# Kernel tuning notes

Hardware: AMD Instinct MI355X
Metric: run time of the kernel (lower is better)

Reference implementation:

```python
import jax, jax.numpy as jnp
import numpy as np

N_NODES = 100000

def _sage_conv(x, src, dst, W_l, b_l, W_r):
    # PyG SAGEConv(aggr='mean'): out = lin_l(mean_{j in N(i)} x_j) + lin_r(x_i)
    agg = jax.ops.segment_sum(x[src], dst, num_segments=N_NODES)          # [N, F]
    cnt = jax.ops.segment_sum(jnp.ones_like(dst, dtype=x.dtype), dst,
                              num_segments=N_NODES)                        # [N]
    mean = agg / jnp.maximum(cnt, 1.0)[:, None]
    return mean @ W_l + b_l + x @ W_r

def setup_inputs() -> dict:
    key = jax.random.key(0)
    ks = jax.random.split(key, 10)
    F_in, H = 128, 16
    E, P = 1600000, 2000000
    x = jax.random.normal(ks[0], (N_NODES, F_in), dtype=jnp.float32)
    edge_index = jax.random.randint(ks[1], (2, E), 0, N_NODES, dtype=jnp.int64)
    decode_index = jax.random.randint(ks[2], (2, P), 0, N_NODES, dtype=jnp.int64)
    s1 = 1.0 / np.sqrt(F_in)
    s2 = 1.0 / np.sqrt(H)
    W1l = jax.random.uniform(ks[3], (F_in, H), jnp.float32, -s1, s1)
    b1 = jax.random.uniform(ks[4], (H,), jnp.float32, -s1, s1)
    W1r = jax.random.uniform(ks[5], (F_in, H), jnp.float32, -s1, s1)
    W2l = jax.random.uniform(ks[6], (H, H), jnp.float32, -s2, s2)
    b2 = jax.random.uniform(ks[7], (H,), jnp.float32, -s2, s2)
    W2r = jax.random.uniform(ks[8], (H, H), jnp.float32, -s2, s2)
    return {"x": x, "W1l": W1l, "b1": b1, "W1r": W1r,
            "W2l": W2l, "b2": b2, "W2r": W2r,
            "edge_index": edge_index, "decode_index": decode_index}

def reference(x, W1l, b1, W1r, W2l, b2, W2r, edge_index, decode_index):
    src, dst = edge_index[0], edge_index[1]
    h = _sage_conv(x, src, dst, W1l, b1, W1r)          # conv1
    h = jax.nn.relu(h)                                  # relu (dropout: eval -> identity)
    h = _sage_conv(h, src, dst, W2l, b2, W2r)           # conv2
    logits = jnp.sum(h[decode_index[0]] * h[decode_index[1]], axis=1)  # [P]
    return jax.nn.sigmoid(logits)
```

## Files before the change

### kernel.cpp

```cpp
#include <hip/hip_runtime.h>
#include <hip/hip_fp16.h>

#define N_NODES 100000
#define F_IN 128
#define H 16
#define NBIN 1563
#define BINCAP 1280
#define ECHUNK 8192
#define QSCALE 4096.0f
#define QINV (1.0f / 4096.0f)

__device__ inline unsigned int packi16(float a, float b) {
  int ia = __float2int_rn(fminf(fmaxf(a * QSCALE, -32767.f), 32767.f));
  int ib = __float2int_rn(fminf(fmaxf(b * QSCALE, -32767.f), 32767.f));
  return (unsigned int)((ia & 0xffff) | (ib << 16));
}

__device__ inline unsigned long long pk64(unsigned int w) {
  return ((unsigned long long)((w >> 16) ^ 0x8000u) << 32)
       | (unsigned long long)((w & 0xffffu) ^ 0x8000u);
}

__global__ void __launch_bounds__(512) k_init(int* __restrict__ binCur) {
  int i = blockIdx.x * 512 + threadIdx.x;
  if (i < NBIN) binCur[i] = i * BINCAP;
}

__global__ void __launch_bounds__(512) k_front(
    const float* __restrict__ x, const float* __restrict__ W1l,
    const float* __restrict__ W1r, unsigned short* __restrict__ y1l,
    float* __restrict__ y1r,
    const int* __restrict__ src, const int* __restrict__ dst,
    int* __restrict__ binCur, int* __restrict__ recs, int E, int fillB) {
  __shared__ __align__(16) char smem[49152];
  int t = threadIdx.x;
  int b = blockIdx.x;
  if (b < fillB) {
    int* hist = (int*)smem;
    int* gbase = hist + NBIN;
    int* cnt2 = gbase + NBIN;
    for (int bb = t; bb < NBIN; bb += 512) { hist[bb] = 0; cnt2[bb] = 0; }
    __syncthreads();
    int base = b * ECHUNK;
    int rec[16], bin[16];
#pragma unroll
    for (int j = 0; j < 16; ++j) {
      int e = base + j * 512 + t;
      if (e < E) {
        int s = src[e];
        int d = dst[e];
        rec[j] = (s << 6) | (d & 63);
        bin[j] = d >> 6;
        atomicAdd(&hist[bin[j]], 1);
      } else {
        bin[j] = -1;
      }
    }
    __syncthreads();
    for (int bb = t; bb < NBIN; bb += 512) {
      int c = hist[bb];
      if (c > 0) gbase[bb] = atomicAdd(&binCur[bb], c);
    }
    __syncthreads();
#pragma unroll
    for (int j = 0; j < 16; ++j) {
      if (bin[j] >= 0) {
        int loc = atomicAdd(&cnt2[bin[j]], 1);
        int slot = gbase[bin[j]] + loc;
        if (slot < (bin[j] + 1) * BINCAP)
          recs[slot] = rec[j];
      }
    }
  } else {
    int lb = b - fillB;
    int wid = __builtin_amdgcn_readfirstlane(t >> 6);
    int part = wid & 3;
    int g = wid >> 2;
    int ln = t & 63;
    int n = lb * 128 + g * 64 + ln;
    int nc = (n < N_NODES) ? n : (N_NODES - 1);
    float* red = (float*)smem + g * 6144;
    const float4* xr = (const float4*)(x + (size_t)nc * F_IN + part * (F_IN / 4));
    float4 xv[8];
#pragma unroll
    for (int j = 0; j < 8; ++j) xv[j] = xr[j];
    const float* Wl = W1l + part * (F_IN / 4) * H;
    const float* Wr = W1r + part * (F_IN / 4) * H;
    float al[H], ar[H];
#pragma unroll
    for (int c = 0; c < H; ++c) { al[c] = 0.f; ar[c] = 0.f; }
#pragma unroll
    for (int j = 0; j < 8; ++j) {
      float xs[4] = {xv[j].x, xv[j].y, xv[j].z, xv[j].w};
#pragma unroll
      for (int jj = 0; jj < 4; ++jj) {
        int k = j * 4 + jj;
#pragma unroll
        for (int c = 0; c < H; ++c) {
          al[c] = fmaf(xs[jj], Wl[k * H + c], al[c]);
          ar[c] = fmaf(xs[jj], Wr[k * H + c], ar[c]);
        }
      }
    }
    if (part != 0) {
      int base = (part - 1) * 2048;
#pragma unroll
      for (int c = 0; c < H; ++c) {
        red[base + c * 64 + ln] = al[c];
        red[base + (H + c) * 64 + ln] = ar[c];
      }
    }
    __syncthreads();
    if (part == 0 && n < N_NODES) {
#pragma unroll
      for (int c = 0; c < H; ++c) {
        al[c] = ((al[c] + red[c * 64 + ln]) + red[2048 + c * 64 + ln])
                + red[4096 + c * 64 + ln];
        ar[c] = ((ar[c] + red[(H + c) * 64 + ln]) + red[2048 + (H + c) * 64 + ln])
                + red[4096 + (H + c) * 64 + ln];
      }
      uint4 w0, w1;
      w0.x = packi16(al[0], al[1]);  w0.y = packi16(al[2], al[3]);
      w0.z = packi16(al[4], al[5]);  w0.w = packi16(al[6], al[7]);
      w1.x = packi16(al[8], al[9]);  w1.y = packi16(al[10], al[11]);
      w1.z = packi16(al[12], al[13]); w1.w = packi16(al[14], al[15]);
      uint4* ol = (uint4*)(y1l + (size_t)n * H);
      ol[0] = w0;
      ol[1] = w1;
      float4* orr = (float4*)(y1r + (size_t)n * H);
#pragma unroll
      for (int q = 0; q < 4; ++q)
        orr[q] = make_float4(ar[4 * q], ar[4 * q + 1], ar[4 * q + 2], ar[4 * q + 3]);
    }
  }
}

__global__ void __launch_bounds__(512) k_agg1(
    const int* __restrict__ recs, const int* __restrict__ binCur,
    const unsigned short* __restrict__ y1l, const float* __restrict__ y1r,
    const float* __restrict__ b1, const float* __restrict__ W2l,
    const float* __restrict__ W2r, unsigned short* __restrict__ z2l,
    float* __restrict__ z2r) {
  __shared__ unsigned long long acc[8][64];
  __shared__ int cnt[64];
  __shared__ float hf[16][64];
  __shared__ float w2l[256];
  __shared__ float w2r[256];
  int t = threadIdx.x;
  int b = blockIdx.x;
  ((unsigned long long*)acc)[t] = 0ULL;
  if (t < 64) cnt[t] = 0;
  if (t < 256) w2l[t] = W2l[t];
  else         w2r[t - 256] = W2r[t - 256];
  __syncthreads();
  int rbase = b * BINCAP;
  int R = binCur[b] - rbase;
  if (R > BINCAP) R = BINCAP;
  int rc[3];
  uint4 va[3], vb[3];
#pragma unroll
  for (int j = 0; j < 3; ++j) {
    int idx = j * 512 + t;
    rc[j] = (idx < R) ? recs[rbase + idx] : -1;
  }
#pragma unroll
  for (int j = 0; j < 3; ++j) {
    int s = (rc[j] >= 0) ? (rc[j] >> 6) : 0;
    const uint4* yp = (const uint4*)(y1l + (size_t)s * H);
    va[j] = yp[0];
    vb[j] = yp[1];
  }
#pragma unroll
  for (int j = 0; j < 3; ++j) {
    if (rc[j] >= 0) {
      int nb = rc[j] & 63;
      atomicAdd(&cnt[nb], 1);
      atomicAdd(&acc[0][nb], pk64(va[j].x));
      atomicAdd(&acc[1][nb], pk64(va[j].y));
      atomicAdd(&acc[2][nb], pk64(va[j].z));
      atomicAdd(&acc[3][nb], pk64(va[j].w));
      atomicAdd(&acc[4][nb], pk64(vb[j].x));
      atomicAdd(&acc[5][nb], pk64(vb[j].y));
      atomicAdd(&acc[6][nb], pk64(vb[j].z));
      atomicAdd(&acc[7][nb], pk64(vb[j].w));
    }
  }
  __syncthreads();
  int node = t >> 3;
  int q = t & 7;
  int n = b * 64 + node;
  float h0 = 0.f, h1 = 0.f;
  if (n < N_NODES) {
    int dg = cnt[node];
    unsigned int bias = (unsigned int)dg << 15;
    float s = QINV / fmaxf((float)dg, 1.f);
    float2 yr = *(const float2*)(y1r + (size_t)n * H + 2 * q);
    float2 bb = *(const float2*)(b1 + 2 * q);
    unsigned long long a = acc[q][node];
    int i0 = (int)((unsigned int)a - bias);
    int i1 = (int)((unsigned int)(a >> 32) - bias);
    h0 = fmaxf(fmaf((float)i0, s, bb.x + yr.x), 0.f);
    h1 = fmaxf(fmaf((float)i1, s, bb.y + yr.y), 0.f);
  }
  hf[2 * q][node] = h0;
  hf[2 * q + 1][node] = h1;
  __syncthreads();
  float zl0 = 0.f, zl1 = 0.f, zr0 = 0.f, zr1 = 0.f;
#pragma unroll
  for (int k = 0; k < 16; ++k) {
    float hk = hf[k][node];
    zl0 = fmaf(hk, w2l[k * 16 + 2 * q], zl0);
    zl1 = fmaf(hk, w2l[k * 16 + 2 * q + 1], zl1);
    zr0 = fmaf(hk, w2r[k * 16 + 2 * q], zr0);
    zr1 = fmaf(hk, w2r[k * 16 + 2 * q + 1], zr1);
  }
  if (n < N_NODES) {
    *(unsigned int*)(z2l + (size_t)n * H + 2 * q) = packi16(zl0, zl1);
    *(float2*)(z2r + (size_t)n * H + 2 * q) = make_float2(zr0, zr1);
  }
}

__global__ void __launch_bounds__(512) k_agg2(
    const int* __restrict__ recs, const int* __restrict__ binCur,
    const unsigned short* __restrict__ z2l, const float* __restrict__ z2r,
    const float* __restrict__ b2, __half* __restrict__ h2) {
  __shared__ unsigned long long acc[8][64];
  __shared__ int cnt[64];
  int t = threadIdx.x;
  int b = blockIdx.x;
  ((unsigned long long*)acc)[t] = 0ULL;
  if (t < 64) cnt[t] = 0;
  __syncthreads();
  int rbase = b * BINCAP;
  int R = binCur[b] - rbase;
  if (R > BINCAP) R = BINCAP;
  int rc[3];
  uint4 va[3], vb[3];
#pragma unroll
  for (int j = 0; j < 3; ++j) {
    int idx = j * 512 + t;
    rc[j] = (idx < R) ? recs[rbase + idx] : -1;
  }
#pragma unroll
  for (int j = 0; j < 3; ++j) {
    int s = (rc[j] >= 0) ? (rc[j] >> 6) : 0;
    const uint4* yp = (const uint4*)(z2l + (size_t)s * H);
    va[j] = yp[0];
    vb[j] = yp[1];
  }
#pragma unroll
  for (int j = 0; j < 3; ++j) {
    if (rc[j] >= 0) {
      int nb = rc[j] & 63;
      atomicAdd(&cnt[nb], 1);
      atomicAdd(&acc[0][nb], pk64(va[j].x));
      atomicAdd(&acc[1][nb], pk64(va[j].y));
      atomicAdd(&acc[2][nb], pk64(va[j].z));
      atomicAdd(&acc[3][nb], pk64(va[j].w));
      atomicAdd(&acc[4][nb], pk64(vb[j].x));
      atomicAdd(&acc[5][nb], pk64(vb[j].y));
      atomicAdd(&acc[6][nb], pk64(vb[j].z));
      atomicAdd(&acc[7][nb], pk64(vb[j].w));
    }
  }
  __syncthreads();
  int node = t >> 3;
  int q = t & 7;
  int n = b * 64 + node;
  if (n < N_NODES) {
    int dg = cnt[node];
    unsigned int bias = (unsigned int)dg << 15;
    float s = QINV / fmaxf((float)dg, 1.f);
    float2 zr = *(const float2*)(z2r + (size_t)n * H + 2 * q);
    float2 bb = *(const float2*)(b2 + 2 * q);
    unsigned long long a = acc[q][node];
    int i0 = (int)((unsigned int)a - bias);
    int i1 = (int)((unsigned int)(a >> 32) - bias);
    float v0 = fmaf((float)i0, s, bb.x + zr.x);
    float v1 = fmaf((float)i1, s, bb.y + zr.y);
    __half2 hh = __floats2half2_rn(v0, v1);
    *(unsigned int*)(h2 + (size_t)n * H + 2 * q) = *(unsigned int*)&hh;
  }
}

__device__ inline float dot8h(uint4 u, uint4 v) {
  float acc = 0.f;
  const unsigned int* uw = (const unsigned int*)&u;
  const unsigned int* vw = (const unsigned int*)&v;
#pragma unroll
  for (int j = 0; j < 4; ++j) {
    float2 a = __half22float2(*(const __half2*)&uw[j]);
    float2 b = __half22float2(*(const __half2*)&vw[j]);
    acc = fmaf(a.x, b.x, acc);
    acc = fmaf(a.y, b.y, acc);
  }
  return acc;
}

__global__ void __launch_bounds__(256) k_decode(
    const int* __restrict__ ps, const int* __restrict__ pd,
    const __half* __restrict__ h2, float* __restrict__ out, int P) {
  int t = blockIdx.x * 256 + threadIdx.x;
  int p = t * 4;
  if (p >= P) return;
  if (p + 3 < P) {
    int4 av = *(const int4*)(ps + p);
    int4 bv = *(const int4*)(pd + p);
    const int an[4] = {av.x, av.y, av.z, av.w};
    const int bn[4] = {bv.x, bv.y, bv.z, bv.w};
    uint4 ua[4][2], ub[4][2];
#pragma unroll
    for (int j = 0; j < 4; ++j) {
      const uint4* ha = (const uint4*)(h2 + (size_t)an[j] * H);
      const uint4* hb = (const uint4*)(h2 + (size_t)bn[j] * H);
      ua[j][0] = ha[0]; ua[j][1] = ha[1];
      ub[j][0] = hb[0]; ub[j][1] = hb[1];
    }
    float4 o;
    float d;
    d = dot8h(ua[0][0], ub[0][0]) + dot8h(ua[0][1], ub[0][1]);
    o.x = 1.f / (1.f + __expf(-d));
    d = dot8h(ua[1][0], ub[1][0]) + dot8h(ua[1][1], ub[1][1]);
    o.y = 1.f / (1.f + __expf(-d));
    d = dot8h(ua[2][0], ub[2][0]) + dot8h(ua[2][1], ub[2][1]);
    o.z = 1.f / (1.f + __expf(-d));
    d = dot8h(ua[3][0], ub[3][0]) + dot8h(ua[3][1], ub[3][1]);
    o.w = 1.f / (1.f + __expf(-d));
    *(float4*)(out + p) = o;
  } else {
    for (int k = 0; k < 4 && p + k < P; ++k) {
      int a = ps[p + k];
      int b = pd[p + k];
      const uint4* ha = (const uint4*)(h2 + (size_t)a * H);
      const uint4* hb = (const uint4*)(h2 + (size_t)b * H);
      float d = dot8h(ha[0], hb[0]) + dot8h(ha[1], hb[1]);
      out[p + k] = 1.f / (1.f + __expf(-d));
    }
  }
}

extern "C" void kernel_launch(void* const* d_in, const int* in_sizes, int n_in,
                              void* d_out, int out_size, void* d_ws, size_t ws_size,
                              hipStream_t stream) {
  const float* x   = (const float*)d_in[0];
  const float* W1l = (const float*)d_in[1];
  const float* b1  = (const float*)d_in[2];
  const float* W1r = (const float*)d_in[3];
  const float* W2l = (const float*)d_in[4];
  const float* b2  = (const float*)d_in[5];
  const float* W2r = (const float*)d_in[6];
  const int* ei = (const int*)d_in[7];
  const int* di = (const int*)d_in[8];
  const int E = in_sizes[7] / 2;
  const int P = in_sizes[8] / 2;

  const size_t NF = (size_t)N_NODES * H;
  unsigned short* y1l = (unsigned short*)d_ws;
  __half*         h2  = (__half*)y1l;
  unsigned short* z2l = y1l + NF;
  float*  y1r = (float*)(z2l + NF);
  float*  z2r = y1r;
  int* recs   = (int*)(y1r + NF);
  int* binCur = recs + (size_t)NBIN * BINCAP;

  const int fillB = (E + ECHUNK - 1) / ECHUNK;
  const int lin1B = (N_NODES + 127) / 128;
  const int initB = (NBIN + 511) / 512;
  const int decodeBlocks = ((P + 3) / 4 + 255) / 256;

  k_init<<<initB, 512, 0, stream>>>(binCur);
  k_front<<<fillB + lin1B, 512, 0, stream>>>(x, W1l, W1r, y1l, y1r,
                                             ei, ei + E, binCur, recs, E, fillB);
  k_agg1<<<NBIN, 512, 0, stream>>>(recs, binCur, y1l, y1r, b1, W2l, W2r,
                                   z2l, z2r);
  k_agg2<<<NBIN, 512, 0, stream>>>(recs, binCur, z2l, z2r, b2, h2);
  k_decode<<<decodeBlocks, 256, 0, stream>>>(di, di + P, h2, (float*)d_out, P);
}
```

Baseline: 197.2 us.

## Shrink front blocks, stage x through swizzled LDS, privatize aggregation atomics

```diff
diff --git a/kernel.cpp b/kernel.cpp
--- a/kernel.cpp
+++ b/kernel.cpp
@@ -6,7 +6,7 @@
 #define H 16
 #define NBIN 1563
 #define BINCAP 1280
-#define ECHUNK 8192
+#define ECHUNK 4096
 #define QSCALE 4096.0f
 #define QINV (1.0f / 4096.0f)
 
@@ -26,26 +26,26 @@
   if (i < NBIN) binCur[i] = i * BINCAP;
 }
 
-__global__ void __launch_bounds__(512) k_front(
+__global__ void __launch_bounds__(256) k_front(
     const float* __restrict__ x, const float* __restrict__ W1l,
     const float* __restrict__ W1r, unsigned short* __restrict__ y1l,
     float* __restrict__ y1r,
     const int* __restrict__ src, const int* __restrict__ dst,
     int* __restrict__ binCur, int* __restrict__ recs, int E, int fillB) {
-  __shared__ __align__(16) char smem[49152];
+  __shared__ __align__(16) char smem[32768];
   int t = threadIdx.x;
   int b = blockIdx.x;
   if (b < fillB) {
     int* hist = (int*)smem;
     int* gbase = hist + NBIN;
     int* cnt2 = gbase + NBIN;
-    for (int bb = t; bb < NBIN; bb += 512) { hist[bb] = 0; cnt2[bb] = 0; }
+    for (int bb = t; bb < NBIN; bb += 256) { hist[bb] = 0; cnt2[bb] = 0; }
     __syncthreads();
     int base = b * ECHUNK;
     int rec[16], bin[16];
 #pragma unroll
     for (int j = 0; j < 16; ++j) {
-      int e = base + j * 512 + t;
+      int e = base + j * 256 + t;
       if (e < E) {
         int s = src[e];
         int d = dst[e];
@@ -57,7 +57,7 @@
       }
     }
     __syncthreads();
-    for (int bb = t; bb < NBIN; bb += 512) {
+    for (int bb = t; bb < NBIN; bb += 256) {
       int c = hist[bb];
       if (c > 0) gbase[bb] = atomicAdd(&binCur[bb], c);
     }
@@ -73,17 +73,28 @@
     }
   } else {
     int lb = b - fillB;
-    int wid = __builtin_amdgcn_readfirstlane(t >> 6);
-    int part = wid & 3;
-    int g = wid >> 2;
+    int part = __builtin_amdgcn_readfirstlane(t >> 6);
     int ln = t & 63;
-    int n = lb * 128 + g * 64 + ln;
-    int nc = (n < N_NODES) ? n : (N_NODES - 1);
-    float* red = (float*)smem + g * 6144;
-    const float4* xr = (const float4*)(x + (size_t)nc * F_IN + part * (F_IN / 4));
+    float4* xs = (float4*)smem;
+    const float4* xg = (const float4*)x;
+    size_t rowbase = (size_t)lb * 64;
+#pragma unroll
+    for (int i = 0; i < 8; ++i) {
+      int f = i * 256 + t;
+      int r = f >> 5;
+      int c = f & 31;
+      size_t rg = rowbase + r;
+      if (rg >= N_NODES) rg = N_NODES - 1;
+      xs[r * 32 + (c ^ (r & 7))] = xg[rg * 32 + c];
+    }
+    __syncthreads();
     float4 xv[8];
-#pragma unroll
-    for (int j = 0; j < 8; ++j) xv[j] = xr[j];
+    int l7 = ln & 7;
+#pragma unroll
+    for (int j = 0; j < 8; ++j)
+      xv[j] = xs[ln * 32 + part * 8 + (j ^ l7)];
+    __syncthreads();
+    int n = lb * 64 + ln;
     const float* Wl = W1l + part * (F_IN / 4) * H;
     const float* Wr = W1r + part * (F_IN / 4) * H;
     float al[H], ar[H];
@@ -91,17 +102,18 @@
     for (int c = 0; c < H; ++c) { al[c] = 0.f; ar[c] = 0.f; }
 #pragma unroll
     for (int j = 0; j < 8; ++j) {
-      float xs[4] = {xv[j].x, xv[j].y, xv[j].z, xv[j].w};
+      float xsv[4] = {xv[j].x, xv[j].y, xv[j].z, xv[j].w};
 #pragma unroll
       for (int jj = 0; jj < 4; ++jj) {
         int k = j * 4 + jj;
 #pragma unroll
         for (int c = 0; c < H; ++c) {
-          al[c] = fmaf(xs[jj], Wl[k * H + c], al[c]);
-          ar[c] = fmaf(xs[jj], Wr[k * H + c], ar[c]);
+          al[c] = fmaf(xsv[jj], Wl[k * H + c], al[c]);
+          ar[c] = fmaf(xsv[jj], Wr[k * H + c], ar[c]);
         }
       }
     }
+    float* red = (float*)smem;
     if (part != 0) {
       int base = (part - 1) * 2048;
 #pragma unroll
@@ -141,21 +153,22 @@
     const float* __restrict__ b1, const float* __restrict__ W2l,
     const float* __restrict__ W2r, unsigned short* __restrict__ z2l,
     float* __restrict__ z2r) {
-  __shared__ unsigned long long acc[8][64];
-  __shared__ int cnt[64];
+  __shared__ unsigned long long acc[4][8][64];
+  __shared__ int cnt4[4][64];
   __shared__ float hf[16][64];
   __shared__ float w2l[256];
   __shared__ float w2r[256];
   int t = threadIdx.x;
   int b = blockIdx.x;
-  ((unsigned long long*)acc)[t] = 0ULL;
-  if (t < 64) cnt[t] = 0;
-  if (t < 256) w2l[t] = W2l[t];
+#pragma unroll
+  for (int j = 0; j < 4; ++j) ((unsigned long long*)acc)[j * 512 + t] = 0ULL;
+  if (t < 256) { ((int*)cnt4)[t] = 0; w2l[t] = W2l[t]; }
   else         w2r[t - 256] = W2r[t - 256];
   __syncthreads();
   int rbase = b * BINCAP;
   int R = binCur[b] - rbase;
   if (R > BINCAP) R = BINCAP;
+  int cp = t & 3;
   int rc[3];
   uint4 va[3], vb[3];
 #pragma unroll
@@ -174,16 +187,25 @@
   for (int j = 0; j < 3; ++j) {
     if (rc[j] >= 0) {
       int nb = rc[j] & 63;
-      atomicAdd(&cnt[nb], 1);
-      atomicAdd(&acc[0][nb], pk64(va[j].x));
-      atomicAdd(&acc[1][nb], pk64(va[j].y));
-      atomicAdd(&acc[2][nb], pk64(va[j].z));
-      atomicAdd(&acc[3][nb], pk64(va[j].w));
-      atomicAdd(&acc[4][nb], pk64(vb[j].x));
-      atomicAdd(&acc[5][nb], pk64(vb[j].y));
-      atomicAdd(&acc[6][nb], pk64(vb[j].z));
-      atomicAdd(&acc[7][nb], pk64(vb[j].w));
-    }
+      atomicAdd(&cnt4[cp][nb], 1);
+      atomicAdd(&acc[cp][0][nb], pk64(va[j].x));
+      atomicAdd(&acc[cp][1][nb], pk64(va[j].y));
+      atomicAdd(&acc[cp][2][nb], pk64(va[j].z));
+      atomicAdd(&acc[cp][3][nb], pk64(va[j].w));
+      atomicAdd(&acc[cp][4][nb], pk64(vb[j].x));
+      atomicAdd(&acc[cp][5][nb], pk64(vb[j].y));
+      atomicAdd(&acc[cp][6][nb], pk64(vb[j].z));
+      atomicAdd(&acc[cp][7][nb], pk64(vb[j].w));
+    }
+  }
+  __syncthreads();
+  {
+    int p = t >> 6;
+    int nd = t & 63;
+    acc[0][p][nd] = ((acc[0][p][nd] + acc[1][p][nd]) + acc[2][p][nd])
+                    + acc[3][p][nd];
+    if (t < 64)
+      cnt4[0][t] = ((cnt4[0][t] + cnt4[1][t]) + cnt4[2][t]) + cnt4[3][t];
   }
   __syncthreads();
   int node = t >> 3;
@@ -191,12 +213,12 @@
   int n = b * 64 + node;
   float h0 = 0.f, h1 = 0.f;
   if (n < N_NODES) {
-    int dg = cnt[node];
+    int dg = cnt4[0][node];
     unsigned int bias = (unsigned int)dg << 15;
     float s = QINV / fmaxf((float)dg, 1.f);
     float2 yr = *(const float2*)(y1r + (size_t)n * H + 2 * q);
     float2 bb = *(const float2*)(b1 + 2 * q);
-    unsigned long long a = acc[q][node];
+    unsigned long long a = acc[0][q][node];
     int i0 = (int)((unsigned int)a - bias);
     int i1 = (int)((unsigned int)(a >> 32) - bias);
     h0 = fmaxf(fmaf((float)i0, s, bb.x + yr.x), 0.f);
@@ -224,16 +246,18 @@
     const int* __restrict__ recs, const int* __restrict__ binCur,
     const unsigned short* __restrict__ z2l, const float* __restrict__ z2r,
     const float* __restrict__ b2, __half* __restrict__ h2) {
-  __shared__ unsigned long long acc[8][64];
-  __shared__ int cnt[64];
+  __shared__ unsigned long long acc[4][8][64];
+  __shared__ int cnt4[4][64];
   int t = threadIdx.x;
   int b = blockIdx.x;
-  ((unsigned long long*)acc)[t] = 0ULL;
-  if (t < 64) cnt[t] = 0;
+#pragma unroll
+  for (int j = 0; j < 4; ++j) ((unsigned long long*)acc)[j * 512 + t] = 0ULL;
+  if (t < 256) ((int*)cnt4)[t] = 0;
   __syncthreads();
   int rbase = b * BINCAP;
   int R = binCur[b] - rbase;
   if (R > BINCAP) R = BINCAP;
+  int cp = t & 3;
   int rc[3];
   uint4 va[3], vb[3];
 #pragma unroll
@@ -252,28 +276,37 @@
   for (int j = 0; j < 3; ++j) {
     if (rc[j] >= 0) {
       int nb = rc[j] & 63;
-      atomicAdd(&cnt[nb], 1);
-      atomicAdd(&acc[0][nb], pk64(va[j].x));
-      atomicAdd(&acc[1][nb], pk64(va[j].y));
-      atomicAdd(&acc[2][nb], pk64(va[j].z));
-      atomicAdd(&acc[3][nb], pk64(va[j].w));
-      atomicAdd(&acc[4][nb], pk64(vb[j].x));
-      atomicAdd(&acc[5][nb], pk64(vb[j].y));
-      atomicAdd(&acc[6][nb], pk64(vb[j].z));
-      atomicAdd(&acc[7][nb], pk64(vb[j].w));
-    }
+      atomicAdd(&cnt4[cp][nb], 1);
+      atomicAdd(&acc[cp][0][nb], pk64(va[j].x));
+      atomicAdd(&acc[cp][1][nb], pk64(va[j].y));
+      atomicAdd(&acc[cp][2][nb], pk64(va[j].z));
+      atomicAdd(&acc[cp][3][nb], pk64(va[j].w));
+      atomicAdd(&acc[cp][4][nb], pk64(vb[j].x));
+      atomicAdd(&acc[cp][5][nb], pk64(vb[j].y));
+      atomicAdd(&acc[cp][6][nb], pk64(vb[j].z));
+      atomicAdd(&acc[cp][7][nb], pk64(vb[j].w));
+    }
+  }
+  __syncthreads();
+  {
+    int p = t >> 6;
+    int nd = t & 63;
+    acc[0][p][nd] = ((acc[0][p][nd] + acc[1][p][nd]) + acc[2][p][nd])
+                    + acc[3][p][nd];
+    if (t < 64)
+      cnt4[0][t] = ((cnt4[0][t] + cnt4[1][t]) + cnt4[2][t]) + cnt4[3][t];
   }
   __syncthreads();
   int node = t >> 3;
   int q = t & 7;
   int n = b * 64 + node;
   if (n < N_NODES) {
-    int dg = cnt[node];
+    int dg = cnt4[0][node];
     unsigned int bias = (unsigned int)dg << 15;
     float s = QINV / fmaxf((float)dg, 1.f);
     float2 zr = *(const float2*)(z2r + (size_t)n * H + 2 * q);
     float2 bb = *(const float2*)(b2 + 2 * q);
-    unsigned long long a = acc[q][node];
+    unsigned long long a = acc[0][q][node];
     int i0 = (int)((unsigned int)a - bias);
     int i1 = (int)((unsigned int)(a >> 32) - bias);
     float v0 = fmaf((float)i0, s, bb.x + zr.x);
@@ -364,12 +397,12 @@
   int* binCur = recs + (size_t)NBIN * BINCAP;
 
   const int fillB = (E + ECHUNK - 1) / ECHUNK;
-  const int lin1B = (N_NODES + 127) / 128;
+  const int lin1B = (N_NODES + 63) / 64;
   const int initB = (NBIN + 511) / 512;
   const int decodeBlocks = ((P + 3) / 4 + 255) / 256;
 
   k_init<<<initB, 512, 0, stream>>>(binCur);
-  k_front<<<fillB + lin1B, 512, 0, stream>>>(x, W1l, W1r, y1l, y1r,
+  k_front<<<fillB + lin1B, 256, 0, stream>>>(x, W1l, W1r, y1l, y1r,
                                              ei, ei + E, binCur, recs, E, fillB);
   k_agg1<<<NBIN, 512, 0, stream>>>(recs, binCur, y1l, y1r, b1, W2l, W2r,
                                    z2l, z2r);
```

New measurement: 204.0 us. +3.4%, slower.

## Replace 64-node bin scatter with per-node fixed-capacity adjacency and gather aggregation

Applied to the files above, without the earlier changes.

```diff
diff --git a/kernel.cpp b/kernel.cpp
--- a/kernel.cpp
+++ b/kernel.cpp
@@ -4,8 +4,7 @@
 #define N_NODES 100000
 #define F_IN 128
 #define H 16
-#define NBIN 1563
-#define BINCAP 1280
+#define NODECAP 64
 #define ECHUNK 8192
 #define QSCALE 4096.0f
 #define QINV (1.0f / 4096.0f)
@@ -16,14 +15,9 @@
   return (unsigned int)((ia & 0xffff) | (ib << 16));
 }
 
-__device__ inline unsigned long long pk64(unsigned int w) {
-  return ((unsigned long long)((w >> 16) ^ 0x8000u) << 32)
-       | (unsigned long long)((w & 0xffffu) ^ 0x8000u);
-}
-
-__global__ void __launch_bounds__(512) k_init(int* __restrict__ binCur) {
+__global__ void __launch_bounds__(512) k_init(int* __restrict__ deg) {
   int i = blockIdx.x * 512 + threadIdx.x;
-  if (i < NBIN) binCur[i] = i * BINCAP;
+  if (i < N_NODES) deg[i] = 0;
 }
 
 __global__ void __launch_bounds__(512) k_front(
@@ -31,44 +25,21 @@
     const float* __restrict__ W1r, unsigned short* __restrict__ y1l,
     float* __restrict__ y1r,
     const int* __restrict__ src, const int* __restrict__ dst,
-    int* __restrict__ binCur, int* __restrict__ recs, int E, int fillB) {
-  __shared__ __align__(16) char smem[49152];
+    int* __restrict__ deg, int* __restrict__ recs2, int E, int fillB) {
+  __shared__ float red2[2][6144];
   int t = threadIdx.x;
   int b = blockIdx.x;
   if (b < fillB) {
-    int* hist = (int*)smem;
-    int* gbase = hist + NBIN;
-    int* cnt2 = gbase + NBIN;
-    for (int bb = t; bb < NBIN; bb += 512) { hist[bb] = 0; cnt2[bb] = 0; }
-    __syncthreads();
     int base = b * ECHUNK;
-    int rec[16], bin[16];
 #pragma unroll
     for (int j = 0; j < 16; ++j) {
       int e = base + j * 512 + t;
       if (e < E) {
         int s = src[e];
         int d = dst[e];
-        rec[j] = (s << 6) | (d & 63);
-        bin[j] = d >> 6;
-        atomicAdd(&hist[bin[j]], 1);
-      } else {
-        bin[j] = -1;
-      }
-    }
-    __syncthreads();
-    for (int bb = t; bb < NBIN; bb += 512) {
-      int c = hist[bb];
-      if (c > 0) gbase[bb] = atomicAdd(&binCur[bb], c);
-    }
-    __syncthreads();
-#pragma unroll
-    for (int j = 0; j < 16; ++j) {
-      if (bin[j] >= 0) {
-        int loc = atomicAdd(&cnt2[bin[j]], 1);
-        int slot = gbase[bin[j]] + loc;
-        if (slot < (bin[j] + 1) * BINCAP)
-          recs[slot] = rec[j];
+        int slot = atomicAdd(&deg[d], 1);
+        if (slot < NODECAP)
+          recs2[(size_t)d * NODECAP + slot] = s;
       }
     }
   } else {
@@ -79,7 +50,7 @@
     int ln = t & 63;
     int n = lb * 128 + g * 64 + ln;
     int nc = (n < N_NODES) ? n : (N_NODES - 1);
-    float* red = (float*)smem + g * 6144;
+    float* red = red2[g];
     const float4* xr = (const float4*)(x + (size_t)nc * F_IN + part * (F_IN / 4));
     float4 xv[8];
 #pragma unroll
@@ -136,71 +107,51 @@
 }
 
 __global__ void __launch_bounds__(512) k_agg1(
-    const int* __restrict__ recs, const int* __restrict__ binCur,
+    const int* __restrict__ recs2, const int* __restrict__ deg,
     const unsigned short* __restrict__ y1l, const float* __restrict__ y1r,
     const float* __restrict__ b1, const float* __restrict__ W2l,
     const float* __restrict__ W2r, unsigned short* __restrict__ z2l,
     float* __restrict__ z2r) {
-  __shared__ unsigned long long acc[8][64];
-  __shared__ int cnt[64];
   __shared__ float hf[16][64];
   __shared__ float w2l[256];
   __shared__ float w2r[256];
   int t = threadIdx.x;
   int b = blockIdx.x;
-  ((unsigned long long*)acc)[t] = 0ULL;
-  if (t < 64) cnt[t] = 0;
   if (t < 256) w2l[t] = W2l[t];
   else         w2r[t - 256] = W2r[t - 256];
-  __syncthreads();
-  int rbase = b * BINCAP;
-  int R = binCur[b] - rbase;
-  if (R > BINCAP) R = BINCAP;
-  int rc[3];
-  uint4 va[3], vb[3];
-#pragma unroll
-  for (int j = 0; j < 3; ++j) {
-    int idx = j * 512 + t;
-    rc[j] = (idx < R) ? recs[rbase + idx] : -1;
-  }
-#pragma unroll
-  for (int j = 0; j < 3; ++j) {
-    int s = (rc[j] >= 0) ? (rc[j] >> 6) : 0;
-    const uint4* yp = (const uint4*)(y1l + (size_t)s * H);
-    va[j] = yp[0];
-    vb[j] = yp[1];
-  }
-#pragma unroll
-  for (int j = 0; j < 3; ++j) {
-    if (rc[j] >= 0) {
-      int nb = rc[j] & 63;
-      atomicAdd(&cnt[nb], 1);
-      atomicAdd(&acc[0][nb], pk64(va[j].x));
-      atomicAdd(&acc[1][nb], pk64(va[j].y));
-      atomicAdd(&acc[2][nb], pk64(va[j].z));
-      atomicAdd(&acc[3][nb], pk64(va[j].w));
-      atomicAdd(&acc[4][nb], pk64(vb[j].x));
-      atomicAdd(&acc[5][nb], pk64(vb[j].y));
-      atomicAdd(&acc[6][nb], pk64(vb[j].z));
-      atomicAdd(&acc[7][nb], pk64(vb[j].w));
-    }
-  }
-  __syncthreads();
   int node = t >> 3;
   int q = t & 7;
   int n = b * 64 + node;
+  int nc = (n < N_NODES) ? n : (N_NODES - 1);
+  int dg = deg[nc];
+  int rl = (n < N_NODES) ? ((dg < NODECAP) ? dg : NODECAP) : 0;
+  const int* run = recs2 + (size_t)nc * NODECAP;
+  int sv[8];
+#pragma unroll
+  for (int k = 0; k < 8; ++k)
+    sv[k] = (k * 8 < rl) ? run[q + k * 8] : 0;
+  int a0 = 0, a1 = 0;
+#pragma unroll
+  for (int k = 0; k < 8; ++k) {
+    if (k * 8 >= rl) break;
+    int sk = sv[k];
+#pragma unroll
+    for (int j = 0; j < 8; ++j) {
+      if (k * 8 + j < rl) {
+        int s = __shfl(sk, j, 8);
+        unsigned int w = *(const unsigned int*)(y1l + (size_t)s * H + 2 * q);
+        a0 += ((int)(w << 16)) >> 16;
+        a1 += ((int)w) >> 16;
+      }
+    }
+  }
   float h0 = 0.f, h1 = 0.f;
   if (n < N_NODES) {
-    int dg = cnt[node];
-    unsigned int bias = (unsigned int)dg << 15;
-    float s = QINV / fmaxf((float)dg, 1.f);
+    float s = QINV / fmaxf((float)rl, 1.f);
     float2 yr = *(const float2*)(y1r + (size_t)n * H + 2 * q);
     float2 bb = *(const float2*)(b1 + 2 * q);
-    unsigned long long a = acc[q][node];
-    int i0 = (int)((unsigned int)a - bias);
-    int i1 = (int)((unsigned int)(a >> 32) - bias);
-    h0 = fmaxf(fmaf((float)i0, s, bb.x + yr.x), 0.f);
-    h1 = fmaxf(fmaf((float)i1, s, bb.y + yr.y), 0.f);
+    h0 = fmaxf(fmaf((float)a0, s, bb.x + yr.x), 0.f);
+    h1 = fmaxf(fmaf((float)a1, s, bb.y + yr.y), 0.f);
   }
   hf[2 * q][node] = h0;
   hf[2 * q + 1][node] = h1;
@@ -221,63 +172,43 @@
 }
 
 __global__ void __launch_bounds__(512) k_agg2(
-    const int* __restrict__ recs, const int* __restrict__ binCur,
+    const int* __restrict__ recs2, const int* __restrict__ deg,
     const unsigned short* __restrict__ z2l, const float* __restrict__ z2r,
     const float* __restrict__ b2, __half* __restrict__ h2) {
-  __shared__ unsigned long long acc[8][64];
-  __shared__ int cnt[64];
   int t = threadIdx.x;
   int b = blockIdx.x;
-  ((unsigned long long*)acc)[t] = 0ULL;
-  if (t < 64) cnt[t] = 0;
-  __syncthreads();
-  int rbase = b * BINCAP;
-  int R = binCur[b] - rbase;
-  if (R > BINCAP) R = BINCAP;
-  int rc[3];
-  uint4 va[3], vb[3];
-#pragma unroll
-  for (int j = 0; j < 3; ++j) {
-    int idx = j * 512 + t;
-    rc[j] = (idx < R) ? recs[rbase + idx] : -1;
-  }
-#pragma unroll
-  for (int j = 0; j < 3; ++j) {
-    int s = (rc[j] >= 0) ? (rc[j] >> 6) : 0;
-    const uint4* yp = (const uint4*)(z2l + (size_t)s * H);
-    va[j] = yp[0];
-    vb[j] = yp[1];
-  }
-#pragma unroll
-  for (int j = 0; j < 3; ++j) {
-    if (rc[j] >= 0) {
-      int nb = rc[j] & 63;
-      atomicAdd(&cnt[nb], 1);
-      atomicAdd(&acc[0][nb], pk64(va[j].x));
-      atomicAdd(&acc[1][nb], pk64(va[j].y));
-      atomicAdd(&acc[2][nb], pk64(va[j].z));
-      atomicAdd(&acc[3][nb], pk64(va[j].w));
-      atomicAdd(&acc[4][nb], pk64(vb[j].x));
-      atomicAdd(&acc[5][nb], pk64(vb[j].y));
-      atomicAdd(&acc[6][nb], pk64(vb[j].z));
-      atomicAdd(&acc[7][nb], pk64(vb[j].w));
-    }
-  }
-  __syncthreads();
   int node = t >> 3;
   int q = t & 7;
   int n = b * 64 + node;
+  int nc = (n < N_NODES) ? n : (N_NODES - 1);
+  int dg = deg[nc];
+  int rl = (n < N_NODES) ? ((dg < NODECAP) ? dg : NODECAP) : 0;
+  const int* run = recs2 + (size_t)nc * NODECAP;
+  int sv[8];
+#pragma unroll
+  for (int k = 0; k < 8; ++k)
+    sv[k] = (k * 8 < rl) ? run[q + k * 8] : 0;
+  int a0 = 0, a1 = 0;
+#pragma unroll
+  for (int k = 0; k < 8; ++k) {
+    if (k * 8 >= rl) break;
+    int sk = sv[k];
+#pragma unroll
+    for (int j = 0; j < 8; ++j) {
+      if (k * 8 + j < rl) {
+        int s = __shfl(sk, j, 8);
+        unsigned int w = *(const unsigned int*)(z2l + (size_t)s * H + 2 * q);
+        a0 += ((int)(w << 16)) >> 16;
+        a1 += ((int)w) >> 16;
+      }
+    }
+  }
   if (n < N_NODES) {
-    int dg = cnt[node];
-    unsigned int bias = (unsigned int)dg << 15;
-    float s = QINV / fmaxf((float)dg, 1.f);
+    float s = QINV / fmaxf((float)rl, 1.f);
     float2 zr = *(const float2*)(z2r + (size_t)n * H + 2 * q);
     float2 bb = *(const float2*)(b2 + 2 * q);
-    unsigned long long a = acc[q][node];
-    int i0 = (int)((unsigned int)a - bias);
-    int i1 = (int)((unsigned int)(a >> 32) - bias);
-    float v0 = fmaf((float)i0, s, bb.x + zr.x);
-    float v1 = fmaf((float)i1, s, bb.y + zr.y);
+    float v0 = fmaf((float)a0, s, bb.x + zr.x);
+    float v1 = fmaf((float)a1, s, bb.y + zr.y);
     __half2 hh = __floats2half2_rn(v0, v1);
     *(unsigned int*)(h2 + (size_t)n * H + 2 * q) = *(unsigned int*)&hh;
   }
@@ -360,19 +291,20 @@
   unsigned short* z2l = y1l + NF;
   float*  y1r = (float*)(z2l + NF);
   float*  z2r = y1r;
-  int* recs   = (int*)(y1r + NF);
-  int* binCur = recs + (size_t)NBIN * BINCAP;
+  int* recs2  = (int*)(y1r + NF);
+  int* deg    = recs2 + (size_t)N_NODES * NODECAP;
 
   const int fillB = (E + ECHUNK - 1) / ECHUNK;
   const int lin1B = (N_NODES + 127) / 128;
-  const int initB = (NBIN + 511) / 512;
+  const int nodeB = (N_NODES + 63) / 64;
+  const int initB = (N_NODES + 511) / 512;
   const int decodeBlocks = ((P + 3) / 4 + 255) / 256;
 
-  k_init<<<initB, 512, 0, stream>>>(binCur);
+  k_init<<<initB, 512, 0, stream>>>(deg);
   k_front<<<fillB + lin1B, 512, 0, stream>>>(x, W1l, W1r, y1l, y1r,
-                                             ei, ei + E, binCur, recs, E, fillB);
-  k_agg1<<<NBIN, 512, 0, stream>>>(recs, binCur, y1l, y1r, b1, W2l, W2r,
-                                   z2l, z2r);
-  k_agg2<<<NBIN, 512, 0, stream>>>(recs, binCur, z2l, z2r, b2, h2);
+                                             ei, ei + E, deg, recs2, E, fillB);
+  k_agg1<<<nodeB, 512, 0, stream>>>(recs2, deg, y1l, y1r, b1, W2l, W2r,
+                                    z2l, z2r);
+  k_agg2<<<nodeB, 512, 0, stream>>>(recs2, deg, z2l, z2r, b2, h2);
   k_decode<<<decodeBlocks, 256, 0, stream>>>(di, di + P, h2, (float*)d_out, P);
 }
```

Result: slower. 281.9 us (+42.9%).

## Pack degree count into accumulator high bits and double edge chunk per bin-fill block

Applied to the files above, without the earlier changes.

```diff
diff --git a/kernel.cpp b/kernel.cpp
--- a/kernel.cpp
+++ b/kernel.cpp
@@ -6,7 +6,7 @@
 #define H 16
 #define NBIN 1563
 #define BINCAP 1280
-#define ECHUNK 8192
+#define ECHUNK 16384
 #define QSCALE 4096.0f
 #define QINV (1.0f / 4096.0f)
 
@@ -32,7 +32,7 @@
     float* __restrict__ y1r,
     const int* __restrict__ src, const int* __restrict__ dst,
     int* __restrict__ binCur, int* __restrict__ recs, int E, int fillB) {
-  __shared__ __align__(16) char smem[49152];
+  __shared__ __align__(16) float smem[12288];
   int t = threadIdx.x;
   int b = blockIdx.x;
   if (b < fillB) {
@@ -42,33 +42,28 @@
     for (int bb = t; bb < NBIN; bb += 512) { hist[bb] = 0; cnt2[bb] = 0; }
     __syncthreads();
     int base = b * ECHUNK;
-    int rec[16], bin[16];
-#pragma unroll
-    for (int j = 0; j < 16; ++j) {
+#pragma unroll
+    for (int j = 0; j < 32; ++j) {
+      int e = base + j * 512 + t;
+      if (e < E) atomicAdd(&hist[dst[e] >> 6], 1);
+    }
+    __syncthreads();
+    for (int bb = t; bb < NBIN; bb += 512) {
+      int c = hist[bb];
+      if (c > 0) gbase[bb] = atomicAdd(&binCur[bb], c);
+    }
+    __syncthreads();
+#pragma unroll
+    for (int j = 0; j < 32; ++j) {
       int e = base + j * 512 + t;
       if (e < E) {
         int s = src[e];
         int d = dst[e];
-        rec[j] = (s << 6) | (d & 63);
-        bin[j] = d >> 6;
-        atomicAdd(&hist[bin[j]], 1);
-      } else {
-        bin[j] = -1;
-      }
-    }
-    __syncthreads();
-    for (int bb = t; bb < NBIN; bb += 512) {
-      int c = hist[bb];
-      if (c > 0) gbase[bb] = atomicAdd(&binCur[bb], c);
-    }
-    __syncthreads();
-#pragma unroll
-    for (int j = 0; j < 16; ++j) {
-      if (bin[j] >= 0) {
-        int loc = atomicAdd(&cnt2[bin[j]], 1);
-        int slot = gbase[bin[j]] + loc;
-        if (slot < (bin[j] + 1) * BINCAP)
-          recs[slot] = rec[j];
+        int bin = d >> 6;
+        int loc = atomicAdd(&cnt2[bin], 1);
+        int slot = gbase[bin] + loc;
+        if (slot < (bin + 1) * BINCAP)
+          recs[slot] = (s << 6) | (d & 63);
       }
     }
   } else {
@@ -79,7 +74,7 @@
     int ln = t & 63;
     int n = lb * 128 + g * 64 + ln;
     int nc = (n < N_NODES) ? n : (N_NODES - 1);
-    float* red = (float*)smem + g * 6144;
+    float* red = smem + g * 6144;
     const float4* xr = (const float4*)(x + (size_t)nc * F_IN + part * (F_IN / 4));
     float4 xv[8];
 #pragma unroll
@@ -142,14 +137,12 @@
     const float* __restrict__ W2r, unsigned short* __restrict__ z2l,
     float* __restrict__ z2r) {
   __shared__ unsigned long long acc[8][64];
-  __shared__ int cnt[64];
   __shared__ float hf[16][64];
   __shared__ float w2l[256];
   __shared__ float w2r[256];
   int t = threadIdx.x;
   int b = blockIdx.x;
   ((unsigned long long*)acc)[t] = 0ULL;
-  if (t < 64) cnt[t] = 0;
   if (t < 256) w2l[t] = W2l[t];
   else         w2r[t - 256] = W2r[t - 256];
   __syncthreads();
@@ -174,8 +167,7 @@
   for (int j = 0; j < 3; ++j) {
     if (rc[j] >= 0) {
       int nb = rc[j] & 63;
-      atomicAdd(&cnt[nb], 1);
-      atomicAdd(&acc[0][nb], pk64(va[j].x));
+      atomicAdd(&acc[0][nb], pk64(va[j].x) + (1ULL << 54));
       atomicAdd(&acc[1][nb], pk64(va[j].y));
       atomicAdd(&acc[2][nb], pk64(va[j].z));
       atomicAdd(&acc[3][nb], pk64(va[j].w));
@@ -191,14 +183,14 @@
   int n = b * 64 + node;
   float h0 = 0.f, h1 = 0.f;
   if (n < N_NODES) {
-    int dg = cnt[node];
+    int dg = (int)(acc[0][node] >> 54);
     unsigned int bias = (unsigned int)dg << 15;
     float s = QINV / fmaxf((float)dg, 1.f);
+    unsigned long long a = acc[q][node];
+    int i0 = (int)((unsigned int)a - bias);
+    int i1 = (int)((((unsigned int)(a >> 32)) & 0x3FFFFFu) - bias);
     float2 yr = *(const float2*)(y1r + (size_t)n * H + 2 * q);
     float2 bb = *(const float2*)(b1 + 2 * q);
-    unsigned long long a = acc[q][node];
-    int i0 = (int)((unsigned int)a - bias);
-    int i1 = (int)((unsigned int)(a >> 32) - bias);
     h0 = fmaxf(fmaf((float)i0, s, bb.x + yr.x), 0.f);
     h1 = fmaxf(fmaf((float)i1, s, bb.y + yr.y), 0.f);
   }
@@ -225,11 +217,9 @@
     const unsigned short* __restrict__ z2l, const float* __restrict__ z2r,
     const float* __restrict__ b2, __half* __restrict__ h2) {
   __shared__ unsigned long long acc[8][64];
-  __shared__ int cnt[64];
   int t = threadIdx.x;
   int b = blockIdx.x;
   ((unsigned long long*)acc)[t] = 0ULL;
-  if (t < 64) cnt[t] = 0;
   __syncthreads();
   int rbase = b * BINCAP;
   int R = binCur[b] - rbase;
@@ -252,8 +242,7 @@
   for (int j = 0; j < 3; ++j) {
     if (rc[j] >= 0) {
       int nb = rc[j] & 63;
-      atomicAdd(&cnt[nb], 1);
-      atomicAdd(&acc[0][nb], pk64(va[j].x));
+      atomicAdd(&acc[0][nb], pk64(va[j].x) + (1ULL << 54));
       atomicAdd(&acc[1][nb], pk64(va[j].y));
       atomicAdd(&acc[2][nb], pk64(va[j].z));
       atomicAdd(&acc[3][nb], pk64(va[j].w));
@@ -268,14 +257,14 @@
   int q = t & 7;
   int n = b * 64 + node;
   if (n < N_NODES) {
-    int dg = cnt[node];
+    int dg = (int)(acc[0][node] >> 54);
     unsigned int bias = (unsigned int)dg << 15;
     float s = QINV / fmaxf((float)dg, 1.f);
+    unsigned long long a = acc[q][node];
+    int i0 = (int)((unsigned int)a - bias);
+    int i1 = (int)((((unsigned int)(a >> 32)) & 0x3FFFFFu) - bias);
     float2 zr = *(const float2*)(z2r + (size_t)n * H + 2 * q);
     float2 bb = *(const float2*)(b2 + 2 * q);
-    unsigned long long a = acc[q][node];
-    int i0 = (int)((unsigned int)a - bias);
-    int i1 = (int)((unsigned int)(a >> 32) - bias);
     float v0 = fmaf((float)i0, s, bb.x + zr.x);
     float v1 = fmaf((float)i1, s, bb.y + zr.y);
     __half2 hh = __floats2half2_rn(v0, v1);
```

New measurement: 225.0 us. +14.1%, slower.
